# Kernel tuning notes

Measured on AMD Instinct MI355X. Metric: run time of the kernel, lower is better.

The kernel has to match this reference:

```python
import jax, jax.numpy as jnp
import numpy as np

D = 64        # input_dim (also per-head dim)
H = 8         # num_heads
L = 128       # split_length (block size)
NEG = -1e9


def _causal_mask(n):
    # additive causal mask: 0 on/below diagonal, -1e9 above
    i = jnp.arange(n)
    return jnp.where(i[:, None] >= i[None, :], 0.0, NEG).astype(jnp.float32)


def setup_inputs() -> dict:
    key = jax.random.key(0)
    ks = jax.random.split(key, 11)
    B, S = 4, 8192
    s = 1.0 / np.sqrt(D)
    inp = {
        "Q": jax.random.normal(ks[0], (B, S, D), jnp.float32),
        "K": jax.random.normal(ks[1], (B, S, D), jnp.float32),
        "V": jax.random.normal(ks[2], (B, S, D), jnp.float32),
        "WQ_w": jax.random.normal(ks[3], (H * D, D), jnp.float32) * s,
        "WQ_b": jnp.zeros((H * D,), jnp.float32),
        "WK_w": jax.random.normal(ks[4], (H * D, D), jnp.float32) * s,
        "WK_b": jnp.zeros((H * D,), jnp.float32),
        "WV_w": jax.random.normal(ks[5], (H * D, D), jnp.float32) * s,
        "WV_b": jnp.zeros((H * D,), jnp.float32),
        "W_w": jax.random.normal(ks[6], (D, H * D), jnp.float32) * (1.0 / np.sqrt(H * D)),
        "W_b": jnp.zeros((D,), jnp.float32),
    }
    return inp


def reference(Q, K, V, WQ_w, WQ_b, WK_w, WK_b, WV_w, WV_b, W_w, W_b):
    B, S, _ = Q.shape
    n = S // L  # number of blocks
    scale = 1.0 / jnp.sqrt(jnp.float32(D))

    def split(x, w, b):
        y = x @ w.T + b                              # [B,S,H*D]
        y = y.reshape(B, n, L, H, D)
        return y.transpose(0, 1, 3, 2, 4)            # [B,n,H,L,D]

    rQ = split(Q, WQ_w, WQ_b)
    rK = split(K, WK_w, WK_b)
    rV = split(V, WV_w, WV_b)

    # block-local causal attention
    s_mask = _causal_mask(L)
    Si = jnp.einsum('bnhqd,bnhkd->bnhqk', rQ, rK) * scale + s_mask
    sim = jax.nn.softmax(Si, axis=-1)
    oV = jnp.einsum('bnhqk,bnhkd->bnhqd', sim, rV)   # [B,n,H,L,D]

    # pooled global attention over blocks
    pooling = oV.mean(axis=3).transpose(0, 2, 1, 3)  # [B,H,n,D]
    g_mask = _causal_mask(n)
    g_Si = jnp.einsum('bhqd,bhkd->bhqk', pooling, pooling) * scale + g_mask
    g_sim = jax.nn.softmax(g_Si, axis=-1)
    global_att = jnp.einsum('bhqk,bhkd->bhqd', g_sim, pooling)  # [B,H,n,D]
    global_att = global_att.transpose(0, 2, 1, 3)    # [B,n,H,D]

    # broadcast-add global context to every position in the block
    oV = oV + global_att[:, :, :, None, :]           # [B,n,H,L,D]

    # merge heads then output projection
    merged = oV.transpose(0, 1, 3, 2, 4).reshape(B, S, H * D)
    out = merged @ W_w.T + W_b                       # [B,S,D]
    return out
```

## Files before the change

kernel.cpp:

```cpp
#include <hip/hip_runtime.h>
#include <stdint.h>

typedef float  v4f  __attribute__((ext_vector_type(4)));
typedef __bf16 v8bf __attribute__((ext_vector_type(8)));
typedef __bf16 v4bf __attribute__((ext_vector_type(4)));
typedef unsigned short u16;

#define NEGBIG (-1.0e9f)

static __device__ __forceinline__ uint2 pack4(v4f a){
  v4bf r;
  r[0]=(__bf16)a[0]; r[1]=(__bf16)a[1]; r[2]=(__bf16)a[2]; r[3]=(__bf16)a[3];
  return __builtin_bit_cast(uint2, r);
}
static __device__ __forceinline__ v8bf pack8(float4 a, float4 b){
  v8bf r;
  r[0]=(__bf16)a.x; r[1]=(__bf16)a.y; r[2]=(__bf16)a.z; r[3]=(__bf16)a.w;
  r[4]=(__bf16)b.x; r[5]=(__bf16)b.y; r[6]=(__bf16)b.z; r[7]=(__bf16)b.w;
  return r;
}
static __device__ __forceinline__ v4f mfma16(v8bf a, v8bf b, v4f c){
  return __builtin_amdgcn_mfma_f32_16x16x32_bf16(a, b, c, 0, 0, 0);
}

static __device__ __forceinline__ v8bf bfly(uint2 t0, uint2 t1, int srcA, int srcB, int hi){
  int a0 = __shfl((int)t0.x, srcA), a1 = __shfl((int)t0.y, srcA);
  int b0 = __shfl((int)t1.x, srcA), b1 = __shfl((int)t1.y, srcA);
  int a2 = __shfl((int)t0.x, srcB), a3 = __shfl((int)t0.y, srcB);
  int b2 = __shfl((int)t1.x, srcB), b3 = __shfl((int)t1.y, srcB);
  uint4 r;
  r.x = hi ? (unsigned)b0 : (unsigned)a0;
  r.y = hi ? (unsigned)b1 : (unsigned)a1;
  r.z = hi ? (unsigned)b2 : (unsigned)a2;
  r.w = hi ? (unsigned)b3 : (unsigned)a3;
  return __builtin_bit_cast(v8bf, r);
}

__global__ __launch_bounds__(256) void k_pre(
    const float* __restrict__ WQ, const float* __restrict__ WK,
    const float* __restrict__ WV, const float* __restrict__ Ww,
    u16* __restrict__ wq, u16* __restrict__ wk,
    u16* __restrict__ wv, u16* __restrict__ ww)
{
  const int seg = blockIdx.x >> 5;
  const int idx = ((blockIdx.x & 31)*256 + threadIdx.x)*4;
  const float* s = (seg==0) ? WQ : (seg==1) ? WK : (seg==2) ? WV : Ww;
  u16*       dst = (seg==0) ? wq : (seg==1) ? wk : (seg==2) ? wv : ww;
  float4 v = *(const float4*)(s + idx);
  v4f a; a[0]=v.x; a[1]=v.y; a[2]=v.z; a[3]=v.w;
  *(uint2*)(dst + idx) = pack4(a);
}

#define LDS_RK    0
#define LDS_VT    16384
#define LDS_WS    32768
#define LDS_WW    57344
#define LDS_POOL  73728
#define LDS_BIAS  77824
#define LDS_TOTAL 80896

__global__ __launch_bounds__(512, 4) void k_fused(
    const float* __restrict__ Q, const float* __restrict__ K, const float* __restrict__ V,
    const u16* __restrict__ wqbf, const u16* __restrict__ wkbf,
    const u16* __restrict__ wvbf, const u16* __restrict__ wwbf,
    const float* __restrict__ bQ, const float* __restrict__ bK, const float* __restrict__ bV,
    float* __restrict__ oVW, float* __restrict__ pool)
{
  extern __shared__ char lds[];

  const int bid = blockIdx.x;
  const int hg  = bid & 1;
  const int tile = bid >> 1;
  const int b = tile >> 6, nb = tile & 63;
  const int rowbase = tile * 128;
  const int tid = threadIdx.x;
  const int w = tid >> 6, l = tid & 63;
  const int l15 = l & 15, g = l >> 4;
  const int swz = (l15 & 7) << 4;
  const int srcA = ((l >> 4) & 1) * 32 + l15;
  const int srcB = srcA + 16;
  const int hi_  = l >> 5;
  const float scale = 0.125f;

  auto STAGE = [&](int hn, int wbuf){
    #pragma unroll
    for (int i = 0; i < 4; ++i){
      const int obase = w*4096 + i*1024;
      const int m   = obase >> 13;
      const int row = ((obase & 8191) >> 7) + (l >> 3);
      const int sc  = (l & 7) << 4;
      const char* src;
      int dst;
      if (m == 3){
        src = (const char*)wwbf + row*1024 + hn*128 + (sc ^ ((row & 7) << 4));
        dst = LDS_WW + wbuf*8192 + (obase - 24576);
      } else {
        const u16* basep = (m == 0) ? wqbf : (m == 1) ? wkbf : wvbf;
        src = (const char*)basep + hn*8192 + row*128 + (sc ^ ((row & 7) << 4));
        dst = LDS_WS + obase;
      }
      __builtin_amdgcn_global_load_lds(
          (const __attribute__((address_space(1))) unsigned int*)src,
          (__attribute__((address_space(3))) unsigned int*)(lds + dst),
          16, 0, 0);
    }
  };

  STAGE(hg*4, 0);

  if (tid < 192){
    const int arr = tid >> 6;
    const int idx = (tid & 63) * 4;
    const float* srcb = (arr==0) ? bQ : (arr==1) ? bK : bV;
    *(float4*)(lds + LDS_BIAS + arr*1024 + idx*4) = *(const float4*)(srcb + hg*256 + idx);
  }

  const int xrow = rowbase + w*16 + l15;
  v8bf xq[2], xk[2], xv[2];
  #pragma unroll
  for (int ks = 0; ks < 2; ++ks){
    const float* qp = Q + xrow*64 + ks*32 + g*8;
    const float* kp = K + xrow*64 + ks*32 + g*8;
    const float* vp = V + xrow*64 + ks*32 + g*8;
    xq[ks] = pack8(*(const float4*)qp, *(const float4*)(qp+4));
    xk[ks] = pack8(*(const float4*)kp, *(const float4*)(kp+4));
    xv[ks] = pack8(*(const float4*)vp, *(const float4*)(vp+4));
  }

  __syncthreads();

  v4f acc_out[4];
  #pragma unroll
  for (int mt = 0; mt < 4; ++mt){ v4f z = {0.f,0.f,0.f,0.f}; acc_out[mt] = z; }

  const int q = w*16 + l15;
  const float* bql = (const float*)(lds + LDS_BIAS);
  const float* bkl = bql + 256;
  const float* bvl = bql + 512;

  for (int hi = 0; hi < 4; ++hi){
    const int h  = hg*4 + hi;
    char* wsb = lds + LDS_WS;

    v4f aq[4], ak[4];
    #pragma unroll
    for (int mt = 0; mt < 4; ++mt){
      float4 b4 = *(const float4*)(bql + hi*64 + mt*16 + g*4);
      aq[mt][0]=b4.x; aq[mt][1]=b4.y; aq[mt][2]=b4.z; aq[mt][3]=b4.w;
      float4 c4 = *(const float4*)(bkl + hi*64 + mt*16 + g*4);
      ak[mt][0]=c4.x; ak[mt][1]=c4.y; ak[mt][2]=c4.z; ak[mt][3]=c4.w;
    }
    #pragma unroll
    for (int ks = 0; ks < 2; ++ks){
      #pragma unroll
      for (int mt = 0; mt < 4; ++mt){
        v8bf wqf = *(const v8bf*)(wsb + (mt*16 + l15)*128 + ((ks*64 + g*16) ^ swz));
        aq[mt] = mfma16(wqf, xq[ks], aq[mt]);
      }
      #pragma unroll
      for (int mt = 0; mt < 4; ++mt){
        v8bf wkf = *(const v8bf*)(wsb + 8192 + (mt*16 + l15)*128 + ((ks*64 + g*16) ^ swz));
        ak[mt] = mfma16(wkf, xk[ks], ak[mt]);
      }
    }
    uint2 pq[4];
    #pragma unroll
    for (int mt = 0; mt < 4; ++mt) pq[mt] = pack4(aq[mt]);
    v8bf qf0 = bfly(pq[0], pq[1], srcA, srcB, hi_);
    v8bf qf1 = bfly(pq[2], pq[3], srcA, srcB, hi_);
    #pragma unroll
    for (int mt = 0; mt < 4; ++mt)
      *(uint2*)(lds + LDS_RK + (w*16 + l15)*128 + ((mt*32 + g*8) ^ swz)) = pack4(ak[mt]);

    {
      v4f av[4];
      #pragma unroll
      for (int nt = 0; nt < 4; ++nt){
        float bs = bvl[hi*64 + nt*16 + l15];
        av[nt][0]=bs; av[nt][1]=bs; av[nt][2]=bs; av[nt][3]=bs;
      }
      #pragma unroll
      for (int ks = 0; ks < 2; ++ks)
        #pragma unroll
        for (int nt = 0; nt < 4; ++nt){
          v8bf wvf = *(const v8bf*)(wsb + 16384 + (nt*16 + l15)*128 + ((ks*64 + g*16) ^ swz));
          av[nt] = mfma16(xv[ks], wvf, av[nt]);
        }
      #pragma unroll
      for (int nt = 0; nt < 4; ++nt)
        *(uint2*)(lds + LDS_VT + (nt*16 + l15)*256 + ((w*32 + g*8) ^ swz)) = pack4(av[nt]);
    }

    __syncthreads();

    if (hi < 3) STAGE(h+1, (hi+1)&1);

    if (hi > 0 && tid < 64){
      const float* pr = (const float*)(lds + LDS_POOL + ((hi-1)&1)*2048);
      float s_ = 0.f;
      #pragma unroll
      for (int p = 0; p < 8; ++p) s_ += pr[p*64 + tid];
      pool[(b*8 + h-1)*4096 + nb*64 + tid] = s_ * (1.0f/128.0f);
    }

    float sum = 0.f;
    uint2 pp[8];
    __builtin_amdgcn_s_setprio(1);
    #pragma unroll
    for (int mt = 0; mt < 8; ++mt){
      if (mt > w){ uint2 z; z.x = 0u; z.y = 0u; pp[mt] = z; continue; }
      v4f s4 = {0.f,0.f,0.f,0.f};
      s4 = mfma16(*(const v8bf*)(lds + LDS_RK + (mt*16 + l15)*128 + ((0*64 + g*16) ^ swz)), qf0, s4);
      s4 = mfma16(*(const v8bf*)(lds + LDS_RK + (mt*16 + l15)*128 + ((1*64 + g*16) ^ swz)), qf1, s4);
      v4f e4;
      #pragma unroll
      for (int r = 0; r < 4; ++r){
        const int key = mt*16 + g*4 + r;
        float v_ = (key <= q) ? s4[r]*scale : NEGBIG;
        float p = __expf(v_);
        e4[r] = p;
        sum += p;
      }
      pp[mt] = pack4(e4);
    }
    __builtin_amdgcn_s_setprio(0);
    sum += __shfl_xor(sum, 16);
    sum += __shfl_xor(sum, 32);
    const float inv = 1.0f / sum;

    v4f oa[4];
    #pragma unroll
    for (int mt = 0; mt < 4; ++mt){ v4f z = {0.f,0.f,0.f,0.f}; oa[mt] = z; }
    const int WKn = (w >> 1) + 1;
    __builtin_amdgcn_s_setprio(1);
    #pragma unroll
    for (int ks = 0; ks < 4; ++ks){
      if (ks >= WKn) continue;
      v8bf pf = bfly(pp[2*ks], pp[2*ks+1], srcA, srcB, hi_);
      #pragma unroll
      for (int mt = 0; mt < 4; ++mt){
        v8bf vf = *(const v8bf*)(lds + LDS_VT + (mt*16 + l15)*256 + ((ks*64 + g*16) ^ swz));
        oa[mt] = mfma16(vf, pf, oa[mt]);
      }
    }
    __builtin_amdgcn_s_setprio(0);

    #pragma unroll
    for (int mt = 0; mt < 4; ++mt){
      oa[mt][0]*=inv; oa[mt][1]*=inv; oa[mt][2]*=inv; oa[mt][3]*=inv;
    }

    {
      float* prd = (float*)(lds + LDS_POOL + (hi&1)*2048);
      #pragma unroll
      for (int mt = 0; mt < 4; ++mt){
        v4f v = oa[mt];
        #pragma unroll
        for (int s_ = 1; s_ < 16; s_ <<= 1){
          v[0] += __shfl_xor(v[0], s_);
          v[1] += __shfl_xor(v[1], s_);
          v[2] += __shfl_xor(v[2], s_);
          v[3] += __shfl_xor(v[3], s_);
        }
        if (l15 == 0)
          *(float4*)(prd + w*64 + mt*16 + g*4) = make_float4(v[0], v[1], v[2], v[3]);
      }
    }

    uint2 po[4];
    #pragma unroll
    for (int mt = 0; mt < 4; ++mt) po[mt] = pack4(oa[mt]);
    v8bf of0 = bfly(po[0], po[1], srcA, srcB, hi_);
    v8bf of1 = bfly(po[2], po[3], srcA, srcB, hi_);
    {
      const char* wwb = lds + LDS_WW + (hi&1)*8192;
      #pragma unroll
      for (int ks = 0; ks < 2; ++ks){
        v8bf off = ks ? of1 : of0;
        #pragma unroll
        for (int mt = 0; mt < 4; ++mt){
          v8bf wf = *(const v8bf*)(wwb + (mt*16 + l15)*128 + ((ks*64 + g*16) ^ swz));
          acc_out[mt] = mfma16(wf, off, acc_out[mt]);
        }
      }
    }

    __syncthreads();
  }

  if (tid < 64){
    const float* pr = (const float*)(lds + LDS_POOL + (3&1)*2048);
    float s_ = 0.f;
    #pragma unroll
    for (int p = 0; p < 8; ++p) s_ += pr[p*64 + tid];
    pool[(b*8 + hg*4 + 3)*4096 + nb*64 + tid] = s_ * (1.0f/128.0f);
  }

  #pragma unroll
  for (int mt = 0; mt < 4; ++mt){
    float4 o;
    o.x = acc_out[mt][0]; o.y = acc_out[mt][1];
    o.z = acc_out[mt][2]; o.w = acc_out[mt][3];
    *(float4*)(oVW + hg*2097152 + (rowbase + w*16 + l15)*64 + mt*16 + g*4) = o;
  }
}

__global__ __launch_bounds__(512) void k_final(
    const float* __restrict__ oVW, const float* __restrict__ Ww, const float* __restrict__ Wb,
    const float* __restrict__ pool, float* __restrict__ out)
{
  __shared__ float pl[64*65];
  __shared__ float prow[64];
  __shared__ float grow[8][64];
  __shared__ float gred[8][64];
  __shared__ float gadd[64];

  const int bid = blockIdx.x;
  const int b = bid >> 6, nb = bid & 63;
  const int rowbase = bid * 128;
  const int tid = threadIdx.x;

  for (int h = 0; h < 8; ++h){
    const float* pb = pool + (b*8 + h)*4096;
    {
      const int e = tid*8;
      float4 a0 = *(const float4*)(pb + e);
      float4 a1 = *(const float4*)(pb + e + 4);
      const int k = e >> 6, d = e & 63;
      *(float4*)(&pl[k*65 + d])     = a0;
      *(float4*)(&pl[k*65 + d + 4]) = a1;
    }
    __syncthreads();

    if (tid < 64){
      const int k = tid;
      float dot = 0.f;
      #pragma unroll
      for (int dd = 0; dd < 16; ++dd){
        float4 t  = *(const float4*)(&pl[k*65  + dd*4]);
        float4 qv = *(const float4*)(&pl[nb*65 + dd*4]);
        dot += t.x*qv.x + t.y*qv.y + t.z*qv.z + t.w*qv.w;
      }
      float sv = (k <= nb) ? dot*0.125f : NEGBIG;
      float mx = sv;
      #pragma unroll
      for (int s = 1; s < 64; s <<= 1) mx = fmaxf(mx, __shfl_xor(mx, s));
      float p = __expf(sv - mx);
      float sum = p;
      #pragma unroll
      for (int s = 1; s < 64; s <<= 1) sum += __shfl_xor(sum, s);
      prow[k] = p / sum;
    }
    __syncthreads();

    {
      const int d = tid & 63, kk = tid >> 6;
      float a = 0.f;
      #pragma unroll
      for (int j = 0; j < 8; ++j){
        const int k = kk*8 + j;
        a += prow[k] * pl[k*65 + d];
      }
      gred[kk][d] = a;
    }
    __syncthreads();
    if (tid < 64){
      float a = 0.f;
      #pragma unroll
      for (int p = 0; p < 8; ++p) a += gred[p][tid];
      grow[h][tid] = a;
    }
    __syncthreads();
  }

  {
    const int dout = tid & 63;
    const int h = tid >> 6;
    const float* wr = Ww + dout*512 + h*64;
    const float* gr = &grow[h][0];
    float a = 0.f;
    #pragma unroll
    for (int dd = 0; dd < 16; ++dd){
      float4 g4 = *(const float4*)(gr + dd*4);
      float4 w4 = *(const float4*)(wr + dd*4);
      a += g4.x*w4.x + g4.y*w4.y + g4.z*w4.z + g4.w*w4.w;
    }
    gred[h][dout] = a;
  }
  __syncthreads();
  if (tid < 64){
    float s = Wb[tid];
    #pragma unroll
    for (int p = 0; p < 8; ++p) s += gred[p][tid];
    gadd[tid] = s;
  }
  __syncthreads();

  const int c4 = (tid & 15) * 4;
  float4 ga = *(const float4*)(&gadd[c4]);
  #pragma unroll
  for (int it = 0; it < 4; ++it){
    const int row = it*32 + (tid >> 4);
    const int idx = (rowbase + row)*64 + c4;
    float4 v0 = *(const float4*)(oVW + idx);
    float4 v1 = *(const float4*)(oVW + 2097152 + idx);
    float4 o;
    o.x = v0.x + v1.x + ga.x; o.y = v0.y + v1.y + ga.y;
    o.z = v0.z + v1.z + ga.z; o.w = v0.w + v1.w + ga.w;
    *(float4*)(out + idx) = o;
  }
}


extern "C" void kernel_launch(void* const* d_in, const int* in_sizes, int n_in,
                              void* d_out, int out_size, void* d_ws, size_t ws_size,
                              hipStream_t stream) {
  const float* Q   = (const float*)d_in[0];
  const float* K   = (const float*)d_in[1];
  const float* V   = (const float*)d_in[2];
  const float* WQw = (const float*)d_in[3];
  const float* WQb = (const float*)d_in[4];
  const float* WKw = (const float*)d_in[5];
  const float* WKb = (const float*)d_in[6];
  const float* WVw = (const float*)d_in[7];
  const float* WVb = (const float*)d_in[8];
  const float* Ww  = (const float*)d_in[9];
  const float* Wb  = (const float*)d_in[10];

  char* ws = (char*)d_ws;
  float* oVW  = (float*)(ws + 0);
  float* pool = (float*)(ws + 16777216);
  u16*   wqbf = (u16*)(ws + 17825792);
  u16*   wkbf = (u16*)(ws + 17891328);
  u16*   wvbf = (u16*)(ws + 17956864);
  u16*   wwbf = (u16*)(ws + 18022400);

  float* outp = (float*)d_out;

  k_pre<<<128, 256, 0, stream>>>(WQw, WKw, WVw, Ww, wqbf, wkbf, wvbf, wwbf);
  k_fused<<<512, 512, LDS_TOTAL, stream>>>(Q, K, V, wqbf, wkbf, wvbf, wwbf,
                                           WQb, WKb, WVb, oVW, pool);
  k_final<<<256, 512, 0, stream>>>(oVW, Ww, Wb, pool, outp);
}
```

Before: 87.78 us.

## Parallelize global attention across heads per wave and relax fused kernel occupancy

The final kernel now assigns one wave per head, computing pooled global attention directly from global memory without the per-head LDS staging loop and its barriers, and sums only over causal keys. The fused kernel's launch-bounds occupancy hint drops from 4 to 2, giving the compiler more registers. The per-wave causal skipping in the score and PV loops is removed and the softmax sum is split into four accumulators, so every wave now does full MFMA work. That simplifies control flow and may help scheduling, but adds redundant compute on masked tiles.

```diff
diff --git a/kernel.cpp b/kernel.cpp
--- a/kernel.cpp
+++ b/kernel.cpp
@@ -59,7 +59,7 @@
 #define LDS_BIAS  77824
 #define LDS_TOTAL 80896
 
-__global__ __launch_bounds__(512, 4) void k_fused(
+__global__ __launch_bounds__(512, 2) void k_fused(
     const float* __restrict__ Q, const float* __restrict__ K, const float* __restrict__ V,
     const u16* __restrict__ wqbf, const u16* __restrict__ wkbf,
     const u16* __restrict__ wvbf, const u16* __restrict__ wwbf,
@@ -203,27 +203,28 @@
       pool[(b*8 + h-1)*4096 + nb*64 + tid] = s_ * (1.0f/128.0f);
     }
 
-    float sum = 0.f;
+    float sm0 = 0.f, sm1 = 0.f, sm2 = 0.f, sm3 = 0.f;
     uint2 pp[8];
     __builtin_amdgcn_s_setprio(1);
     #pragma unroll
     for (int mt = 0; mt < 8; ++mt){
-      if (mt > w){ uint2 z; z.x = 0u; z.y = 0u; pp[mt] = z; continue; }
       v4f s4 = {0.f,0.f,0.f,0.f};
       s4 = mfma16(*(const v8bf*)(lds + LDS_RK + (mt*16 + l15)*128 + ((0*64 + g*16) ^ swz)), qf0, s4);
       s4 = mfma16(*(const v8bf*)(lds + LDS_RK + (mt*16 + l15)*128 + ((1*64 + g*16) ^ swz)), qf1, s4);
       v4f e4;
-      #pragma unroll
-      for (int r = 0; r < 4; ++r){
-        const int key = mt*16 + g*4 + r;
-        float v_ = (key <= q) ? s4[r]*scale : NEGBIG;
-        float p = __expf(v_);
-        e4[r] = p;
-        sum += p;
+      {
+        const int key = mt*16 + g*4;
+        float p0 = __expf((key+0 <= q) ? s4[0]*scale : NEGBIG);
+        float p1 = __expf((key+1 <= q) ? s4[1]*scale : NEGBIG);
+        float p2 = __expf((key+2 <= q) ? s4[2]*scale : NEGBIG);
+        float p3 = __expf((key+3 <= q) ? s4[3]*scale : NEGBIG);
+        e4[0]=p0; e4[1]=p1; e4[2]=p2; e4[3]=p3;
+        sm0 += p0; sm1 += p1; sm2 += p2; sm3 += p3;
       }
       pp[mt] = pack4(e4);
     }
     __builtin_amdgcn_s_setprio(0);
+    float sum = (sm0 + sm1) + (sm2 + sm3);
     sum += __shfl_xor(sum, 16);
     sum += __shfl_xor(sum, 32);
     const float inv = 1.0f / sum;
@@ -231,11 +232,9 @@
     v4f oa[4];
     #pragma unroll
     for (int mt = 0; mt < 4; ++mt){ v4f z = {0.f,0.f,0.f,0.f}; oa[mt] = z; }
-    const int WKn = (w >> 1) + 1;
     __builtin_amdgcn_s_setprio(1);
     #pragma unroll
     for (int ks = 0; ks < 4; ++ks){
-      if (ks >= WKn) continue;
       v8bf pf = bfly(pp[2*ks], pp[2*ks+1], srcA, srcB, hi_);
       #pragma unroll
       for (int mt = 0; mt < 4; ++mt){
@@ -309,8 +308,7 @@
     const float* __restrict__ oVW, const float* __restrict__ Ww, const float* __restrict__ Wb,
     const float* __restrict__ pool, float* __restrict__ out)
 {
-  __shared__ float pl[64*65];
-  __shared__ float prow[64];
+  __shared__ float prow[8][64];
   __shared__ float grow[8][64];
   __shared__ float gred[8][64];
   __shared__ float gadd[64];
@@ -319,79 +317,50 @@
   const int b = bid >> 6, nb = bid & 63;
   const int rowbase = bid * 128;
   const int tid = threadIdx.x;
-
-  for (int h = 0; h < 8; ++h){
-    const float* pb = pool + (b*8 + h)*4096;
-    {
-      const int e = tid*8;
-      float4 a0 = *(const float4*)(pb + e);
-      float4 a1 = *(const float4*)(pb + e + 4);
-      const int k = e >> 6, d = e & 63;
-      *(float4*)(&pl[k*65 + d])     = a0;
-      *(float4*)(&pl[k*65 + d + 4]) = a1;
-    }
-    __syncthreads();
-
-    if (tid < 64){
-      const int k = tid;
-      float dot = 0.f;
-      #pragma unroll
-      for (int dd = 0; dd < 16; ++dd){
-        float4 t  = *(const float4*)(&pl[k*65  + dd*4]);
-        float4 qv = *(const float4*)(&pl[nb*65 + dd*4]);
-        dot += t.x*qv.x + t.y*qv.y + t.z*qv.z + t.w*qv.w;
-      }
-      float sv = (k <= nb) ? dot*0.125f : NEGBIG;
-      float mx = sv;
-      #pragma unroll
-      for (int s = 1; s < 64; s <<= 1) mx = fmaxf(mx, __shfl_xor(mx, s));
-      float p = __expf(sv - mx);
-      float sum = p;
-      #pragma unroll
-      for (int s = 1; s < 64; s <<= 1) sum += __shfl_xor(sum, s);
-      prow[k] = p / sum;
-    }
-    __syncthreads();
-
-    {
-      const int d = tid & 63, kk = tid >> 6;
-      float a = 0.f;
-      #pragma unroll
-      for (int j = 0; j < 8; ++j){
-        const int k = kk*8 + j;
-        a += prow[k] * pl[k*65 + d];
-      }
-      gred[kk][d] = a;
-    }
-    __syncthreads();
-    if (tid < 64){
-      float a = 0.f;
-      #pragma unroll
-      for (int p = 0; p < 8; ++p) a += gred[p][tid];
-      grow[h][tid] = a;
-    }
-    __syncthreads();
-  }
+  const int w = tid >> 6, l = tid & 63;
+
+  const float* pb = pool + (b*8 + w)*4096;
+
+  float dot = 0.f;
+  #pragma unroll
+  for (int dd = 0; dd < 16; ++dd){
+    float4 t  = *(const float4*)(pb + l*64  + dd*4);
+    float4 qv = *(const float4*)(pb + nb*64 + dd*4);
+    dot += t.x*qv.x + t.y*qv.y + t.z*qv.z + t.w*qv.w;
+  }
+  float sv = (l <= nb) ? dot*0.125f : NEGBIG;
+  float mx = sv;
+  #pragma unroll
+  for (int s = 1; s < 64; s <<= 1) mx = fmaxf(mx, __shfl_xor(mx, s));
+  float p = __expf(sv - mx);
+  float sum = p;
+  #pragma unroll
+  for (int s = 1; s < 64; s <<= 1) sum += __shfl_xor(sum, s);
+  prow[w][l] = p / sum;
 
   {
-    const int dout = tid & 63;
-    const int h = tid >> 6;
-    const float* wr = Ww + dout*512 + h*64;
-    const float* gr = &grow[h][0];
     float a = 0.f;
+    for (int k = 0; k <= nb; ++k)
+      a += prow[w][k] * pb[k*64 + l];
+    grow[w][l] = a;
+  }
+
+  {
+    const float* wr = Ww + l*512 + w*64;
+    float c = 0.f;
     #pragma unroll
     for (int dd = 0; dd < 16; ++dd){
-      float4 g4 = *(const float4*)(gr + dd*4);
+      float4 g4 = *(const float4*)(&grow[w][dd*4]);
       float4 w4 = *(const float4*)(wr + dd*4);
-      a += g4.x*w4.x + g4.y*w4.y + g4.z*w4.z + g4.w*w4.w;
-    }
-    gred[h][dout] = a;
+      c += g4.x*w4.x + g4.y*w4.y + g4.z*w4.z + g4.w*w4.w;
+    }
+    gred[w][l] = c;
   }
   __syncthreads();
   if (tid < 64){
     float s = Wb[tid];
     #pragma unroll
-    for (int p = 0; p < 8; ++p) s += gred[p][tid];
+    for (int ph = 0; ph < 8; ++ph) s += gred[ph][tid];
     gadd[tid] = s;
   }
   __syncthreads();
```

Result: slower. 99.56 us (+13.4%).
